# Performance work log

Hardware: AMD Instinct MI355X
Metric: run time of the kernel (lower is better)

The kernel has to match this reference:

```python
import jax, jax.numpy as jnp
import numpy as np

TOP_K = 2


def setup_inputs() -> dict:
    key = jax.random.key(0)
    ks = jax.random.split(key, 5)
    B, S, D, E, I = 1, 2048, 2880, 8, 2880
    scale_in = 1.0 / np.sqrt(D)
    scale_mid = 1.0 / np.sqrt(I)
    return {
        "x": jax.random.normal(ks[0], (B, S, D), dtype=jnp.float32),
        "w_router": jax.random.normal(ks[1], (D, E), dtype=jnp.float32) * scale_in,
        "w_gate": jax.random.normal(ks[2], (E, D, I), dtype=jnp.float32) * scale_in,
        "w_up": jax.random.normal(ks[3], (E, D, I), dtype=jnp.float32) * scale_in,
        "w_down": jax.random.normal(ks[4], (E, I, D), dtype=jnp.float32) * scale_mid,
    }


def reference(x, w_router, w_gate, w_up, w_down):
    B, S, D = x.shape
    E = w_router.shape[1]
    t = x.reshape(-1, D)  # [T, D] flattened tokens

    # --- RouterTopK: softmax over experts, then top-k selection ---
    logits = t @ w_router                      # [T, E]
    affinities = jax.nn.softmax(logits, axis=-1)
    top_vals, top_idx = jax.lax.top_k(affinities, TOP_K)   # [T, K]
    # normalize_top_k_affinities=True: renormalize selected weights to sum to 1
    top_vals = top_vals / jnp.sum(top_vals, axis=-1, keepdims=True)

    # scatter normalized weights into dense [T, E] combine matrix
    T = t.shape[0]
    tok = jnp.arange(T)[:, None]
    weights = jnp.zeros((T, E), dtype=t.dtype).at[tok, top_idx].set(top_vals)

    # --- Expert SiLU-GLU MLPs (computed per expert, combined by weights) ---
    gate = jnp.einsum("td,edi->eti", t, w_gate)  # [E, T, I]
    up = jnp.einsum("td,edi->eti", t, w_up)      # [E, T, I]
    h = jax.nn.silu(gate) * up                   # [E, T, I]
    y = jnp.einsum("eti,eid->etd", h, w_down)    # [E, T, D]

    out = jnp.einsum("te,etd->td", weights, y)   # affinity-weighted combine
    return out.reshape(B, S, D)
```

## Files before the change

### kernel.cpp

```cpp
#include <hip/hip_runtime.h>
#include <hip/hip_fp16.h>
#include <stdint.h>
#include <math.h>


typedef _Float16 f16;
typedef _Float16 f16x8 __attribute__((ext_vector_type(8)));
typedef float f32x4 __attribute__((ext_vector_type(4)));

#define T_TOK 2048
#define DDIM 2880
#define NEXP 8
#define IDIM 2880

#define BM 128
#define BN 96
#define BK 64
#define NKT 45
#define NNT 30
#define MAXMT 40
#define NBLK (NNT*MAXMT)
#define SLOT_CAP 5120

#define XH_OFF   0
#define XH_BYTES (T_TOK*DDIM*2)
#define HBUF_OFF (XH_OFF + XH_BYTES)
#define HBUF_BYTES (SLOT_CAP*IDIM*2)
#define YBUF_OFF (HBUF_OFF + HBUF_BYTES)
#define YBUF_BYTES (SLOT_CAP*DDIM*2)
#define META_OFF (YBUF_OFF + YBUF_BYTES)
#define M_COUNT 0
#define M_CUR 8
#define M_OFFS 16
#define M_NTILES 25
#define M_TILE_E 32
#define M_TILE_R0 96
#define M_SLOT_TOK 160
#define M_SLOT_OF (160+SLOT_CAP)
#define M_TOK_E (M_SLOT_OF + 2*T_TOK)
#define META_INTS (M_TOK_E + 2*T_TOK)
#define SLOTW_OFF (META_OFF + META_INTS*4)
#define TOKW_OFF  (SLOTW_OFF + SLOT_CAP*4)
#define WS_NEEDED ((size_t)TOKW_OFF + (size_t)T_TOK*2*4)

__device__ __forceinline__ int swz(int row) { return ((row ^ (row >> 3)) & 7) << 4; }

__device__ __forceinline__ void gload_lds16(const void* gp, void* lp) {
  __builtin_amdgcn_global_load_lds(
      (const __attribute__((address_space(1))) uint32_t*)gp,
      (__attribute__((address_space(3))) uint32_t*)lp,
      16, 0, 0);
}

__global__ __launch_bounds__(256) void k_router(
    const float* __restrict__ x, const float* __restrict__ wr,
    int* __restrict__ meta, float* __restrict__ tok_w) {
  const int lane = threadIdx.x & 63;
  const int t = blockIdx.x * 4 + (threadIdx.x >> 6);
  double acc[NEXP];
#pragma unroll
  for (int e = 0; e < NEXP; e++) acc[e] = 0.0;
  for (int d = lane; d < DDIM; d += 64) {
    float xv = x[(size_t)t * DDIM + d];
    float4 w0 = *(const float4*)(wr + (size_t)d * NEXP);
    float4 w1 = *(const float4*)(wr + (size_t)d * NEXP + 4);
    acc[0] += (double)xv * (double)w0.x;
    acc[1] += (double)xv * (double)w0.y;
    acc[2] += (double)xv * (double)w0.z;
    acc[3] += (double)xv * (double)w0.w;
    acc[4] += (double)xv * (double)w1.x;
    acc[5] += (double)xv * (double)w1.y;
    acc[6] += (double)xv * (double)w1.z;
    acc[7] += (double)xv * (double)w1.w;
  }
#pragma unroll
  for (int m = 32; m >= 1; m >>= 1) {
#pragma unroll
    for (int e = 0; e < NEXP; e++) acc[e] += __shfl_xor(acc[e], m, 64);
  }
  if (lane == 0) {
    int e0 = 0;
#pragma unroll
    for (int e = 1; e < NEXP; e++) if (acc[e] > acc[e0]) e0 = e;
    int e1 = (e0 == 0) ? 1 : 0;
#pragma unroll
    for (int e = 0; e < NEXP; e++) if (e != e0 && acc[e] > acc[e1]) e1 = e;
    double w0 = 1.0 / (1.0 + exp(acc[e1] - acc[e0]));
    meta[M_TOK_E + 2*t]     = e0;
    meta[M_TOK_E + 2*t + 1] = e1;
    tok_w[2*t]     = (float)w0;
    tok_w[2*t + 1] = (float)(1.0 - w0);
    atomicAdd(&meta[M_COUNT + e0], 1);
    atomicAdd(&meta[M_COUNT + e1], 1);
  }
}

__global__ __launch_bounds__(256) void k_xcvt(const float* __restrict__ x, f16* __restrict__ xh) {
  size_t i = ((size_t)blockIdx.x * 256 + threadIdx.x) * 8;
  float4 a = *(const float4*)(x + i);
  float4 b = *(const float4*)(x + i + 4);
  f16x8 v;
  v[0]=(f16)a.x; v[1]=(f16)a.y; v[2]=(f16)a.z; v[3]=(f16)a.w;
  v[4]=(f16)b.x; v[5]=(f16)b.y; v[6]=(f16)b.z; v[7]=(f16)b.w;
  *(f16x8*)(xh + i) = v;
}

__global__ __launch_bounds__(64) void k_scan(int* __restrict__ meta, float* __restrict__ slot_w) {
  __shared__ int s_off[NEXP], s_cnt[NEXP], s_pc[NEXP];
  if (threadIdx.x == 0) {
    int run = 0, nt = 0;
    for (int e = 0; e < NEXP; e++) {
      int c = meta[M_COUNT + e];
      int mt = (c + BM - 1) / BM;
      meta[M_OFFS + e] = run;
      s_off[e] = run; s_cnt[e] = c; s_pc[e] = mt * BM;
      for (int j = 0; j < mt; j++) { meta[M_TILE_E + nt] = e; meta[M_TILE_R0 + nt] = run + j * BM; nt++; }
      run += mt * BM;
      meta[M_CUR + e] = 0;
    }
    meta[M_OFFS + NEXP] = run;
    meta[M_NTILES] = nt;
  }
  __syncthreads();
  for (int e = 0; e < NEXP; e++) {
    for (int i = s_cnt[e] + (int)threadIdx.x; i < s_pc[e]; i += 64) {
      meta[M_SLOT_TOK + s_off[e] + i] = 0;
      slot_w[s_off[e] + i] = 0.0f;
    }
  }
}

__global__ __launch_bounds__(256) void k_scatter(int* __restrict__ meta,
    float* __restrict__ slot_w, const float* __restrict__ tok_w) {
  int t = blockIdx.x * 256 + threadIdx.x;
  if (t >= T_TOK) return;
#pragma unroll
  for (int k = 0; k < 2; k++) {
    int e = meta[M_TOK_E + 2*t + k];
    int pos = atomicAdd(&meta[M_CUR + e], 1);
    int slot = meta[M_OFFS + e] + pos;
    meta[M_SLOT_TOK + slot] = t;
    slot_w[slot] = tok_w[2*t + k];
    meta[M_SLOT_OF + 2*t + k] = slot;
  }
}

__global__ __launch_bounds__(256, 2) void k_gemm1(
    const f16* __restrict__ xh, const float* __restrict__ wg, const float* __restrict__ wu,
    f16* __restrict__ hbuf, const int* __restrict__ meta) {
  const int id = blockIdx.x;
  const int sid = (id & 7) * (NBLK / 8) + (id >> 3);
  const int mt = sid % MAXMT;
  const int nb = sid / MAXMT;
  if (mt >= meta[M_NTILES]) return;
  const int e  = meta[M_TILE_E + mt];
  const int r0 = meta[M_TILE_R0 + mt];
  const int n0 = nb * BN;

  __shared__ ushort sA[2][BM * BK];
  __shared__ ushort sB[2][BN * BK];

  const int tid = threadIdx.x;
  const int lane = tid & 63;
  const int w = tid >> 6;
  const int wm = w >> 1, wn = w & 1;

  const char* a_gbase[4];
  int a_loff[4];
#pragma unroll
  for (int i = 0; i < 4; i++) {
    int seg = w * 4 + i;
    int row = seg * 8 + (lane >> 3);
    int colb = ((lane & 7) * 16) ^ swz(row);
    int tok = meta[M_SLOT_TOK + r0 + row];
    a_gbase[i] = (const char*)(xh + (size_t)tok * DDIM) + colb;
    a_loff[i] = seg * 1024;
  }

  const int bn0 = (tid % 24) * 4;
  const int bk0 = (tid / 24) * 8;
  const bool bact = tid < 192;
  const float* bgbase = wg + ((size_t)e * DDIM + bk0) * IDIM + n0 + bn0;
  const float* bubase = wu + ((size_t)e * DDIM + bk0) * IDIM + n0 + bn0;

  float4 vB[2][8];

  f32x4 accG[4][3], accU[4][3];
#pragma unroll
  for (int i = 0; i < 4; i++)
#pragma unroll
    for (int j = 0; j < 3; j++) { accG[i][j] = {0.f,0.f,0.f,0.f}; accU[i][j] = {0.f,0.f,0.f,0.f}; }

#pragma unroll
  for (int i = 0; i < 4; i++) gload_lds16(a_gbase[i], (char*)sA[0] + a_loff[i]);
  if (bact) {
#pragma unroll
    for (int j = 0; j < 8; j++) vB[0][j] = *(const float4*)(bgbase + (size_t)j * IDIM);
#pragma unroll
    for (int j = 0; j < 8; j++) vB[1][j] = *(const float4*)(bubase + (size_t)j * IDIM);
  }

  for (int kt = 0; kt < NKT; kt++) {
    const int cur = kt & 1;
    __syncthreads();
    if (bact) {
#pragma unroll
      for (int m = 0; m < 2; m++)
#pragma unroll
        for (int c = 0; c < 4; c++) {
          f16x8 p;
#pragma unroll
          for (int j = 0; j < 8; j++) {
            float fc = (c==0) ? vB[m][j].x : (c==1) ? vB[m][j].y : (c==2) ? vB[m][j].z : vB[m][j].w;
            p[j] = (f16)fc;
          }
          *(f16x8*)((char*)sB[m] + (bn0 + c) * 128 + ((bk0 * 2) ^ swz(bn0 + c))) = p;
        }
    }
    __syncthreads();
    if (kt + 1 < NKT) {
#pragma unroll
      for (int i = 0; i < 4; i++)
        gload_lds16(a_gbase[i] + (kt + 1) * 128, (char*)sA[cur ^ 1] + a_loff[i]);
      if (bact) {
        const float* bg = bgbase + (size_t)(kt + 1) * BK * IDIM;
        const float* bu = bubase + (size_t)(kt + 1) * BK * IDIM;
#pragma unroll
        for (int j = 0; j < 8; j++) vB[0][j] = *(const float4*)(bg + (size_t)j * IDIM);
#pragma unroll
        for (int j = 0; j < 8; j++) vB[1][j] = *(const float4*)(bu + (size_t)j * IDIM);
      }
    }
#pragma unroll
    for (int kk = 0; kk < 2; kk++) {
      const int gb = kk * 64 + ((lane >> 4) * 16);
      f16x8 af[4], bg[3], bu[3];
#pragma unroll
      for (int fm = 0; fm < 4; fm++) {
        int row = wm * 64 + fm * 16 + (lane & 15);
        af[fm] = *(const f16x8*)((const char*)sA[cur] + row * 128 + (gb ^ swz(row)));
      }
#pragma unroll
      for (int fn = 0; fn < 3; fn++) {
        int row = wn * 48 + fn * 16 + (lane & 15);
        bg[fn] = *(const f16x8*)((const char*)sB[0] + row * 128 + (gb ^ swz(row)));
        bu[fn] = *(const f16x8*)((const char*)sB[1] + row * 128 + (gb ^ swz(row)));
      }
#pragma unroll
      for (int fm = 0; fm < 4; fm++)
#pragma unroll
        for (int fn = 0; fn < 3; fn++) {
          accG[fm][fn] = __builtin_amdgcn_mfma_f32_16x16x32_f16(af[fm], bg[fn], accG[fm][fn], 0, 0, 0);
          accU[fm][fn] = __builtin_amdgcn_mfma_f32_16x16x32_f16(af[fm], bu[fn], accU[fm][fn], 0, 0, 0);
        }
    }
  }
#pragma unroll
  for (int fm = 0; fm < 4; fm++)
#pragma unroll
    for (int fn = 0; fn < 3; fn++)
#pragma unroll
      for (int j = 0; j < 4; j++) {
        int row = wm * 64 + fm * 16 + ((lane >> 4) * 4) + j;
        int col = n0 + wn * 48 + fn * 16 + (lane & 15);
        float g = accG[fm][fn][j], u = accU[fm][fn][j];
        float h = g * u / (1.0f + __expf(-g));
        hbuf[(size_t)(r0 + row) * IDIM + col] = (f16)h;
      }
}

__global__ __launch_bounds__(256, 3) void k_gemm2(
    const f16* __restrict__ hbuf, const float* __restrict__ wd,
    f16* __restrict__ ybuf, const int* __restrict__ meta, const float* __restrict__ slot_w) {
  const int id = blockIdx.x;
  const int sid = (id & 7) * (NBLK / 8) + (id >> 3);
  const int mt = sid % MAXMT;
  const int nb = sid / MAXMT;
  if (mt >= meta[M_NTILES]) return;
  const int e  = meta[M_TILE_E + mt];
  const int r0 = meta[M_TILE_R0 + mt];
  const int n0 = nb * BN;

  __shared__ ushort sA[2][BM * BK];
  __shared__ ushort sB1[BN * BK];

  const int tid = threadIdx.x;
  const int lane = tid & 63;
  const int w = tid >> 6;
  const int wm = w >> 1, wn = w & 1;

  const char* a_gbase[4];
  int a_loff[4];
#pragma unroll
  for (int i = 0; i < 4; i++) {
    int seg = w * 4 + i;
    int row = seg * 8 + (lane >> 3);
    int colb = ((lane & 7) * 16) ^ swz(row);
    a_gbase[i] = (const char*)(hbuf + (size_t)(r0 + row) * IDIM) + colb;
    a_loff[i] = seg * 1024;
  }

  const int bn0 = (tid % 24) * 4;
  const int bk0 = (tid / 24) * 8;
  const bool bact = tid < 192;
  const float* bdbase = wd + ((size_t)e * IDIM + bk0) * DDIM + n0 + bn0;

  float4 vB[8];

  f32x4 acc[4][3];
#pragma unroll
  for (int i = 0; i < 4; i++)
#pragma unroll
    for (int j = 0; j < 3; j++) acc[i][j] = {0.f,0.f,0.f,0.f};

#pragma unroll
  for (int i = 0; i < 4; i++) gload_lds16(a_gbase[i], (char*)sA[0] + a_loff[i]);
  if (bact) {
#pragma unroll
    for (int j = 0; j < 8; j++) vB[j] = *(const float4*)(bdbase + (size_t)j * DDIM);
  }

  for (int kt = 0; kt < NKT; kt++) {
    const int cur = kt & 1;
    __syncthreads();
    if (bact) {
#pragma unroll
      for (int c = 0; c < 4; c++) {
        f16x8 p;
#pragma unroll
        for (int j = 0; j < 8; j++) {
          float fc = (c==0) ? vB[j].x : (c==1) ? vB[j].y : (c==2) ? vB[j].z : vB[j].w;
          p[j] = (f16)fc;
        }
        *(f16x8*)((char*)sB1 + (bn0 + c) * 128 + ((bk0 * 2) ^ swz(bn0 + c))) = p;
      }
    }
    __syncthreads();
    if (kt + 1 < NKT) {
#pragma unroll
      for (int i = 0; i < 4; i++)
        gload_lds16(a_gbase[i] + (kt + 1) * 128, (char*)sA[cur ^ 1] + a_loff[i]);
      if (bact) {
        const float* bd = bdbase + (size_t)(kt + 1) * BK * DDIM;
#pragma unroll
        for (int j = 0; j < 8; j++) vB[j] = *(const float4*)(bd + (size_t)j * DDIM);
      }
    }
#pragma unroll
    for (int kk = 0; kk < 2; kk++) {
      const int gb = kk * 64 + ((lane >> 4) * 16);
      f16x8 af[4], bf[3];
#pragma unroll
      for (int fm = 0; fm < 4; fm++) {
        int row = wm * 64 + fm * 16 + (lane & 15);
        af[fm] = *(const f16x8*)((const char*)sA[cur] + row * 128 + (gb ^ swz(row)));
      }
#pragma unroll
      for (int fn = 0; fn < 3; fn++) {
        int row = wn * 48 + fn * 16 + (lane & 15);
        bf[fn] = *(const f16x8*)((const char*)sB1 + row * 128 + (gb ^ swz(row)));
      }
#pragma unroll
      for (int fm = 0; fm < 4; fm++)
#pragma unroll
        for (int fn = 0; fn < 3; fn++)
          acc[fm][fn] = __builtin_amdgcn_mfma_f32_16x16x32_f16(af[fm], bf[fn], acc[fm][fn], 0, 0, 0);
    }
  }
#pragma unroll
  for (int fm = 0; fm < 4; fm++)
#pragma unroll
    for (int fn = 0; fn < 3; fn++)
#pragma unroll
      for (int j = 0; j < 4; j++) {
        int row = wm * 64 + fm * 16 + ((lane >> 4) * 4) + j;
        int col = n0 + wn * 48 + fn * 16 + (lane & 15);
        int slot = r0 + row;
        float wv = slot_w[slot];
        ybuf[(size_t)slot * DDIM + col] = (f16)(acc[fm][fn][j] * wv);
      }
}

__global__ __launch_bounds__(256) void k_combine(const f16* __restrict__ ybuf,
    const int* __restrict__ meta, float* __restrict__ out) {
  size_t idx = (size_t)blockIdx.x * 256 + threadIdx.x;
  int t = (int)(idx / (DDIM/8));
  int c = (int)(idx % (DDIM/8));
  int s0 = meta[M_SLOT_OF + 2*t];
  int s1 = meta[M_SLOT_OF + 2*t + 1];
  f16x8 a = *(const f16x8*)(ybuf + (size_t)s0 * DDIM + c*8);
  f16x8 b = *(const f16x8*)(ybuf + (size_t)s1 * DDIM + c*8);
  float4 o0, o1;
  o0.x = (float)a[0] + (float)b[0];
  o0.y = (float)a[1] + (float)b[1];
  o0.z = (float)a[2] + (float)b[2];
  o0.w = (float)a[3] + (float)b[3];
  o1.x = (float)a[4] + (float)b[4];
  o1.y = (float)a[5] + (float)b[5];
  o1.z = (float)a[6] + (float)b[6];
  o1.w = (float)a[7] + (float)b[7];
  float* op = out + (size_t)t * DDIM + c*8;
  *(float4*)op = o0;
  *(float4*)(op + 4) = o1;
}

extern "C" void kernel_launch(void* const* d_in, const int* in_sizes, int n_in,
                              void* d_out, int out_size, void* d_ws, size_t ws_size,
                              hipStream_t stream) {
  const float* x  = (const float*)d_in[0];
  const float* wr = (const float*)d_in[1];
  const float* wg = (const float*)d_in[2];
  const float* wu = (const float*)d_in[3];
  const float* wd = (const float*)d_in[4];
  float* out = (float*)d_out;
  char* ws = (char*)d_ws;
  if (ws_size < WS_NEEDED) return;

  f16* xh    = (f16*)(ws + XH_OFF);
  f16* hbuf  = (f16*)(ws + HBUF_OFF);
  f16* ybuf  = (f16*)(ws + YBUF_OFF);
  int* meta  = (int*)(ws + META_OFF);
  float* slot_w = (float*)(ws + SLOTW_OFF);
  float* tok_w  = (float*)(ws + TOKW_OFF);

  hipMemsetAsync(meta + M_COUNT, 0, NEXP * sizeof(int), stream);
  k_router<<<T_TOK/4, 256, 0, stream>>>(x, wr, meta, tok_w);
  k_xcvt<<<(T_TOK*DDIM/8 + 255)/256, 256, 0, stream>>>(x, xh);
  k_scan<<<1, 64, 0, stream>>>(meta, slot_w);
  k_scatter<<<(T_TOK + 255)/256, 256, 0, stream>>>(meta, slot_w, tok_w);
  k_gemm1<<<NBLK, 256, 0, stream>>>(xh, wg, wu, hbuf, meta);
  k_gemm2<<<NBLK, 256, 0, stream>>>(hbuf, wd, ybuf, meta, slot_w);
  k_combine<<<(T_TOK*DDIM/8 + 255)/256, 256, 0, stream>>>(ybuf, meta, out);
}
```

Measured before the change: 619.7 us.

## Enlarge MoE GEMM tiles to 256 rows with 512-thread blocks

Both expert GEMMs now use 256-row M tiles and 512-thread blocks. In gemm1 each warp pair specialises on either the gate or the up projection, and the up results are exchanged through LDS to apply SiLU-GLU. Gemm2 widens N tiles to 192, and the ybuf now aliases the xh workspace to save memory. The larger tiles cut how often weights are re-read per expert and raise arithmetic intensity, at the cost of more padding waste per expert tile, higher register pressure and an extra LDS exchange epilogue.

```diff
diff --git a/kernel.cpp b/kernel.cpp
--- a/kernel.cpp
+++ b/kernel.cpp
@@ -13,21 +13,24 @@
 #define NEXP 8
 #define IDIM 2880
 
-#define BM 128
-#define BN 96
+#define BM 256
 #define BK 64
 #define NKT 45
-#define NNT 30
-#define MAXMT 40
-#define NBLK (NNT*MAXMT)
-#define SLOT_CAP 5120
-
-#define XH_OFF   0
-#define XH_BYTES (T_TOK*DDIM*2)
-#define HBUF_OFF (XH_OFF + XH_BYTES)
-#define HBUF_BYTES (SLOT_CAP*IDIM*2)
-#define YBUF_OFF (HBUF_OFF + HBUF_BYTES)
-#define YBUF_BYTES (SLOT_CAP*DDIM*2)
+#define BN1 96
+#define NNT1 30
+#define BN2 192
+#define NNT2 15
+#define MAXMT 24
+#define NB1 (NNT1*MAXMT)
+#define NB2 (NNT2*MAXMT)
+#define SLOT_CAP 6144
+
+#define HBUF_OFF 0
+#define HBUF_BYTES ((size_t)SLOT_CAP*IDIM*2)
+#define XH_OFF   (HBUF_OFF + HBUF_BYTES)
+#define XH_BYTES ((size_t)T_TOK*DDIM*2)
+#define YBUF_OFF XH_OFF
+#define YBUF_BYTES ((size_t)SLOT_CAP*DDIM*2)
 #define META_OFF (YBUF_OFF + YBUF_BYTES)
 #define M_COUNT 0
 #define M_CUR 8
@@ -145,25 +148,26 @@
   }
 }
 
-__global__ __launch_bounds__(256, 2) void k_gemm1(
+__global__ __launch_bounds__(512, 2) void k_gemm1(
     const f16* __restrict__ xh, const float* __restrict__ wg, const float* __restrict__ wu,
     f16* __restrict__ hbuf, const int* __restrict__ meta) {
   const int id = blockIdx.x;
-  const int sid = (id & 7) * (NBLK / 8) + (id >> 3);
+  const int sid = (id & 7) * (NB1 / 8) + (id >> 3);
   const int mt = sid % MAXMT;
   const int nb = sid / MAXMT;
   if (mt >= meta[M_NTILES]) return;
   const int e  = meta[M_TILE_E + mt];
   const int r0 = meta[M_TILE_R0 + mt];
-  const int n0 = nb * BN;
+  const int n0 = nb * BN1;
 
   __shared__ ushort sA[2][BM * BK];
-  __shared__ ushort sB[2][BN * BK];
-
-  const int tid = threadIdx.x;
+  __shared__ ushort sB[2][BN1 * BK];
+
+  const int tid  = threadIdx.x;
   const int lane = tid & 63;
-  const int w = tid >> 6;
-  const int wm = w >> 1, wn = w & 1;
+  const int w    = tid >> 6;
+  const int wm   = w >> 1;
+  const int gu   = w & 1;
 
   const char* a_gbase[4];
   int a_loff[4];
@@ -177,27 +181,25 @@
     a_loff[i] = seg * 1024;
   }
 
-  const int bn0 = (tid % 24) * 4;
-  const int bk0 = (tid / 24) * 8;
-  const bool bact = tid < 192;
-  const float* bgbase = wg + ((size_t)e * DDIM + bk0) * IDIM + n0 + bn0;
-  const float* bubase = wu + ((size_t)e * DDIM + bk0) * IDIM + n0 + bn0;
-
-  float4 vB[2][8];
-
-  f32x4 accG[4][3], accU[4][3];
+  const int bm_ = tid / 192;
+  const int tt  = tid % 192;
+  const int bn0 = (tt % 24) * 4;
+  const int bk0 = (tt / 24) * 8;
+  const bool bact = tid < 384;
+  const float* bsrc = (bm_ ? wu : wg) + ((size_t)e * DDIM + bk0) * IDIM + n0 + bn0;
+
+  float4 vB[8];
+  f32x4 acc[4][6];
 #pragma unroll
   for (int i = 0; i < 4; i++)
 #pragma unroll
-    for (int j = 0; j < 3; j++) { accG[i][j] = {0.f,0.f,0.f,0.f}; accU[i][j] = {0.f,0.f,0.f,0.f}; }
+    for (int j = 0; j < 6; j++) acc[i][j] = {0.f,0.f,0.f,0.f};
 
 #pragma unroll
   for (int i = 0; i < 4; i++) gload_lds16(a_gbase[i], (char*)sA[0] + a_loff[i]);
   if (bact) {
 #pragma unroll
-    for (int j = 0; j < 8; j++) vB[0][j] = *(const float4*)(bgbase + (size_t)j * IDIM);
-#pragma unroll
-    for (int j = 0; j < 8; j++) vB[1][j] = *(const float4*)(bubase + (size_t)j * IDIM);
+    for (int j = 0; j < 8; j++) vB[j] = *(const float4*)(bsrc + (size_t)j * IDIM);
   }
 
   for (int kt = 0; kt < NKT; kt++) {
@@ -205,17 +207,15 @@
     __syncthreads();
     if (bact) {
 #pragma unroll
-      for (int m = 0; m < 2; m++)
-#pragma unroll
-        for (int c = 0; c < 4; c++) {
-          f16x8 p;
-#pragma unroll
-          for (int j = 0; j < 8; j++) {
-            float fc = (c==0) ? vB[m][j].x : (c==1) ? vB[m][j].y : (c==2) ? vB[m][j].z : vB[m][j].w;
-            p[j] = (f16)fc;
-          }
-          *(f16x8*)((char*)sB[m] + (bn0 + c) * 128 + ((bk0 * 2) ^ swz(bn0 + c))) = p;
+      for (int c = 0; c < 4; c++) {
+        f16x8 p;
+#pragma unroll
+        for (int j = 0; j < 8; j++) {
+          float fc = (c==0) ? vB[j].x : (c==1) ? vB[j].y : (c==2) ? vB[j].z : vB[j].w;
+          p[j] = (f16)fc;
         }
+        *(f16x8*)((char*)sB[bm_] + (bn0 + c) * 128 + ((bk0 * 2) ^ swz(bn0 + c))) = p;
+      }
     }
     __syncthreads();
     if (kt + 1 < NKT) {
@@ -223,71 +223,87 @@
       for (int i = 0; i < 4; i++)
         gload_lds16(a_gbase[i] + (kt + 1) * 128, (char*)sA[cur ^ 1] + a_loff[i]);
       if (bact) {
-        const float* bg = bgbase + (size_t)(kt + 1) * BK * IDIM;
-        const float* bu = bubase + (size_t)(kt + 1) * BK * IDIM;
-#pragma unroll
-        for (int j = 0; j < 8; j++) vB[0][j] = *(const float4*)(bg + (size_t)j * IDIM);
-#pragma unroll
-        for (int j = 0; j < 8; j++) vB[1][j] = *(const float4*)(bu + (size_t)j * IDIM);
+        const float* bs = bsrc + (size_t)(kt + 1) * BK * IDIM;
+#pragma unroll
+        for (int j = 0; j < 8; j++) vB[j] = *(const float4*)(bs + (size_t)j * IDIM);
       }
     }
 #pragma unroll
     for (int kk = 0; kk < 2; kk++) {
       const int gb = kk * 64 + ((lane >> 4) * 16);
-      f16x8 af[4], bg[3], bu[3];
+      f16x8 af[4], bf[6];
 #pragma unroll
       for (int fm = 0; fm < 4; fm++) {
         int row = wm * 64 + fm * 16 + (lane & 15);
         af[fm] = *(const f16x8*)((const char*)sA[cur] + row * 128 + (gb ^ swz(row)));
       }
 #pragma unroll
-      for (int fn = 0; fn < 3; fn++) {
-        int row = wn * 48 + fn * 16 + (lane & 15);
-        bg[fn] = *(const f16x8*)((const char*)sB[0] + row * 128 + (gb ^ swz(row)));
-        bu[fn] = *(const f16x8*)((const char*)sB[1] + row * 128 + (gb ^ swz(row)));
+      for (int fn = 0; fn < 6; fn++) {
+        int row = fn * 16 + (lane & 15);
+        bf[fn] = *(const f16x8*)((const char*)sB[gu] + row * 128 + (gb ^ swz(row)));
       }
 #pragma unroll
       for (int fm = 0; fm < 4; fm++)
 #pragma unroll
-        for (int fn = 0; fn < 3; fn++) {
-          accG[fm][fn] = __builtin_amdgcn_mfma_f32_16x16x32_f16(af[fm], bg[fn], accG[fm][fn], 0, 0, 0);
-          accU[fm][fn] = __builtin_amdgcn_mfma_f32_16x16x32_f16(af[fm], bu[fn], accU[fm][fn], 0, 0, 0);
-        }
-    }
-  }
-#pragma unroll
-  for (int fm = 0; fm < 4; fm++)
-#pragma unroll
-    for (int fn = 0; fn < 3; fn++)
-#pragma unroll
-      for (int j = 0; j < 4; j++) {
-        int row = wm * 64 + fm * 16 + ((lane >> 4) * 4) + j;
-        int col = n0 + wn * 48 + fn * 16 + (lane & 15);
-        float g = accG[fm][fn][j], u = accU[fm][fn][j];
-        float h = g * u / (1.0f + __expf(-g));
-        hbuf[(size_t)(r0 + row) * IDIM + col] = (f16)h;
-      }
-}
-
-__global__ __launch_bounds__(256, 3) void k_gemm2(
+        for (int fn = 0; fn < 6; fn++)
+          acc[fm][fn] = __builtin_amdgcn_mfma_f32_16x16x32_f16(af[fm], bf[fn], acc[fm][fn], 0, 0, 0);
+    }
+  }
+
+  float* u_lds = (float*)&sA[0][0];
+  const int rl4 = (lane >> 4) * 4;
+  const int cl  = lane & 15;
+#pragma unroll
+  for (int r = 0; r < 2; r++) {
+    __syncthreads();
+    if (gu == 1) {
+#pragma unroll
+      for (int fi = 0; fi < 2; fi++)
+#pragma unroll
+        for (int fn = 0; fn < 6; fn++)
+#pragma unroll
+          for (int j = 0; j < 4; j++)
+            u_lds[wm * 3200 + (fi * 16 + rl4 + j) * 100 + fn * 16 + cl] = acc[2*r + fi][fn][j];
+    }
+    __syncthreads();
+    if (gu == 0) {
+#pragma unroll
+      for (int fi = 0; fi < 2; fi++) {
+        int fm = 2*r + fi;
+#pragma unroll
+        for (int fn = 0; fn < 6; fn++)
+#pragma unroll
+          for (int j = 0; j < 4; j++) {
+            float u = u_lds[wm * 3200 + (fi * 16 + rl4 + j) * 100 + fn * 16 + cl];
+            float g = acc[fm][fn][j];
+            float h = g * u / (1.0f + __expf(-g));
+            hbuf[(size_t)(r0 + wm * 64 + fm * 16 + rl4 + j) * IDIM + n0 + fn * 16 + cl] = (f16)h;
+          }
+      }
+    }
+  }
+}
+
+__global__ __launch_bounds__(512, 2) void k_gemm2(
     const f16* __restrict__ hbuf, const float* __restrict__ wd,
     f16* __restrict__ ybuf, const int* __restrict__ meta, const float* __restrict__ slot_w) {
   const int id = blockIdx.x;
-  const int sid = (id & 7) * (NBLK / 8) + (id >> 3);
+  const int sid = (id & 7) * (NB2 / 8) + (id >> 3);
   const int mt = sid % MAXMT;
   const int nb = sid / MAXMT;
   if (mt >= meta[M_NTILES]) return;
   const int e  = meta[M_TILE_E + mt];
   const int r0 = meta[M_TILE_R0 + mt];
-  const int n0 = nb * BN;
+  const int n0 = nb * BN2;
 
   __shared__ ushort sA[2][BM * BK];
-  __shared__ ushort sB1[BN * BK];
-
-  const int tid = threadIdx.x;
+  __shared__ ushort sB1[BN2 * BK];
+
+  const int tid  = threadIdx.x;
   const int lane = tid & 63;
-  const int w = tid >> 6;
-  const int wm = w >> 1, wn = w & 1;
+  const int w    = tid >> 6;
+  const int wm   = w >> 1;
+  const int wn   = w & 1;
 
   const char* a_gbase[4];
   int a_loff[4];
@@ -300,24 +316,25 @@
     a_loff[i] = seg * 1024;
   }
 
-  const int bn0 = (tid % 24) * 4;
-  const int bk0 = (tid / 24) * 8;
-  const bool bact = tid < 192;
-  const float* bdbase = wd + ((size_t)e * IDIM + bk0) * DDIM + n0 + bn0;
+  const int half = tid / 192;
+  const int tt   = tid % 192;
+  const int bn0  = half * 96 + (tt % 24) * 4;
+  const int bk0  = (tt / 24) * 8;
+  const bool bact = tid < 384;
+  const float* bsrc = wd + ((size_t)e * IDIM + bk0) * DDIM + n0 + bn0;
 
   float4 vB[8];
-
-  f32x4 acc[4][3];
+  f32x4 acc[4][6];
 #pragma unroll
   for (int i = 0; i < 4; i++)
 #pragma unroll
-    for (int j = 0; j < 3; j++) acc[i][j] = {0.f,0.f,0.f,0.f};
+    for (int j = 0; j < 6; j++) acc[i][j] = {0.f,0.f,0.f,0.f};
 
 #pragma unroll
   for (int i = 0; i < 4; i++) gload_lds16(a_gbase[i], (char*)sA[0] + a_loff[i]);
   if (bact) {
 #pragma unroll
-    for (int j = 0; j < 8; j++) vB[j] = *(const float4*)(bdbase + (size_t)j * DDIM);
+    for (int j = 0; j < 8; j++) vB[j] = *(const float4*)(bsrc + (size_t)j * DDIM);
   }
 
   for (int kt = 0; kt < NKT; kt++) {
@@ -341,44 +358,48 @@
       for (int i = 0; i < 4; i++)
         gload_lds16(a_gbase[i] + (kt + 1) * 128, (char*)sA[cur ^ 1] + a_loff[i]);
       if (bact) {
-        const float* bd = bdbase + (size_t)(kt + 1) * BK * DDIM;
-#pragma unroll
-        for (int j = 0; j < 8; j++) vB[j] = *(const float4*)(bd + (size_t)j * DDIM);
+        const float* bs = bsrc + (size_t)(kt + 1) * BK * DDIM;
+#pragma unroll
+        for (int j = 0; j < 8; j++) vB[j] = *(const float4*)(bs + (size_t)j * DDIM);
       }
     }
 #pragma unroll
     for (int kk = 0; kk < 2; kk++) {
       const int gb = kk * 64 + ((lane >> 4) * 16);
-      f16x8 af[4], bf[3];
+      f16x8 af[4], bf[6];
 #pragma unroll
       for (int fm = 0; fm < 4; fm++) {
         int row = wm * 64 + fm * 16 + (lane & 15);
         af[fm] = *(const f16x8*)((const char*)sA[cur] + row * 128 + (gb ^ swz(row)));
       }
 #pragma unroll
-      for (int fn = 0; fn < 3; fn++) {
-        int row = wn * 48 + fn * 16 + (lane & 15);
+      for (int fn = 0; fn < 6; fn++) {
+        int row = wn * 96 + fn * 16 + (lane & 15);
         bf[fn] = *(const f16x8*)((const char*)sB1 + row * 128 + (gb ^ swz(row)));
       }
 #pragma unroll
       for (int fm = 0; fm < 4; fm++)
 #pragma unroll
-        for (int fn = 0; fn < 3; fn++)
+        for (int fn = 0; fn < 6; fn++)
           acc[fm][fn] = __builtin_amdgcn_mfma_f32_16x16x32_f16(af[fm], bf[fn], acc[fm][fn], 0, 0, 0);
     }
   }
+
+  const int rl4 = (lane >> 4) * 4;
+  const int cl  = lane & 15;
 #pragma unroll
   for (int fm = 0; fm < 4; fm++)
 #pragma unroll
-    for (int fn = 0; fn < 3; fn++)
-#pragma unroll
-      for (int j = 0; j < 4; j++) {
-        int row = wm * 64 + fm * 16 + ((lane >> 4) * 4) + j;
-        int col = n0 + wn * 48 + fn * 16 + (lane & 15);
-        int slot = r0 + row;
-        float wv = slot_w[slot];
+    for (int j = 0; j < 4; j++) {
+      int row = wm * 64 + fm * 16 + rl4 + j;
+      int slot = r0 + row;
+      float wv = slot_w[slot];
+#pragma unroll
+      for (int fn = 0; fn < 6; fn++) {
+        int col = n0 + wn * 96 + fn * 16 + cl;
         ybuf[(size_t)slot * DDIM + col] = (f16)(acc[fm][fn][j] * wv);
       }
+    }
 }
 
 __global__ __launch_bounds__(256) void k_combine(const f16* __restrict__ ybuf,
@@ -416,8 +437,8 @@
   char* ws = (char*)d_ws;
   if (ws_size < WS_NEEDED) return;
 
+  f16* hbuf  = (f16*)(ws + HBUF_OFF);
   f16* xh    = (f16*)(ws + XH_OFF);
-  f16* hbuf  = (f16*)(ws + HBUF_OFF);
   f16* ybuf  = (f16*)(ws + YBUF_OFF);
   int* meta  = (int*)(ws + META_OFF);
   float* slot_w = (float*)(ws + SLOTW_OFF);
@@ -428,7 +449,7 @@
   k_xcvt<<<(T_TOK*DDIM/8 + 255)/256, 256, 0, stream>>>(x, xh);
   k_scan<<<1, 64, 0, stream>>>(meta, slot_w);
   k_scatter<<<(T_TOK + 255)/256, 256, 0, stream>>>(meta, slot_w, tok_w);
-  k_gemm1<<<NBLK, 256, 0, stream>>>(xh, wg, wu, hbuf, meta);
-  k_gemm2<<<NBLK, 256, 0, stream>>>(hbuf, wd, ybuf, meta, slot_w);
+  k_gemm1<<<NB1, 512, 0, stream>>>(xh, wg, wu, hbuf, meta);
+  k_gemm2<<<NB2, 512, 0, stream>>>(hbuf, wd, ybuf, meta, slot_w);
   k_combine<<<(T_TOK*DDIM/8 + 255)/256, 256, 0, stream>>>(ybuf, meta, out);
 }
```

Result: slower. 691.3 us (+11.6%).
